# Kernel optimization log

Measured on AMD Instinct MI355X. Metric: run time of the kernel, lower is better.

Reference implementation:

```python
import jax, jax.numpy as jnp
import numpy as np

N_NODES = 50000
N_EDGES = 800000
D = 128
HEADS = 4
HEAD_DIM = D // HEADS
N_LAYERS = 3
NEG_SLOPE = 0.2


def setup_inputs() -> dict:
    key = jax.random.key(0)
    ks = jax.random.split(key, 10)
    x = jax.random.normal(ks[0], (N_NODES, D), dtype=jnp.float32)
    edge_index = jax.random.randint(ks[1], (2, N_EDGES), 0, N_NODES, dtype=jnp.int32)
    s = 1.0 / np.sqrt(D)
    gcn_w = jax.random.normal(ks[2], (N_LAYERS, D, D), dtype=jnp.float32) * s
    gcn_b = jnp.zeros((N_LAYERS, D), dtype=jnp.float32)
    gat_w = jax.random.normal(ks[3], (N_LAYERS, D, D), dtype=jnp.float32) * s
    gat_att_src = jax.random.normal(ks[4], (N_LAYERS, HEADS, HEAD_DIM), dtype=jnp.float32) * s
    gat_att_dst = jax.random.normal(ks[5], (N_LAYERS, HEADS, HEAD_DIM), dtype=jnp.float32) * s
    gat_b = jnp.zeros((N_LAYERS, D), dtype=jnp.float32)
    ln_g = jnp.ones((N_LAYERS, D), dtype=jnp.float32)
    ln_b = jnp.zeros((N_LAYERS, D), dtype=jnp.float32)
    return {"x": x, "edge_index": edge_index, "gcn_w": gcn_w, "gcn_b": gcn_b,
            "gat_w": gat_w, "gat_att_src": gat_att_src, "gat_att_dst": gat_att_dst,
            "gat_b": gat_b, "ln_g": ln_g, "ln_b": ln_b}


def _gcn(x, src, dst, n, w, b):
    # PyG GCNConv: self-loops (already in src/dst), symmetric normalization
    xw = x @ w                                             # [N, D]
    deg = jax.ops.segment_sum(jnp.ones_like(dst, dtype=xw.dtype), dst, num_segments=n)
    dinv = jax.lax.rsqrt(deg)                              # deg >= 1 due to self-loops
    norm = dinv[src] * dinv[dst]                           # [E]
    out = jax.ops.segment_sum(xw[src] * norm[:, None], dst, num_segments=n)
    return out + b


def _gat(x, src, dst, n, w, att_src, att_dst, b):
    # PyG GATConv, concat heads, self-loops already in src/dst
    xw = (x @ w).reshape(n, HEADS, HEAD_DIM)               # [N, H, Dh]
    a_src = (xw * att_src).sum(-1)                         # [N, H]
    a_dst = (xw * att_dst).sum(-1)                         # [N, H]
    e = jax.nn.leaky_relu(a_src[src] + a_dst[dst], NEG_SLOPE)  # [E, H]
    m = jax.ops.segment_max(e, dst, num_segments=n)        # [N, H]
    ee = jnp.exp(e - m[dst])
    z = jax.ops.segment_sum(ee, dst, num_segments=n)       # [N, H]
    alpha = ee / z[dst]                                    # [E, H]
    out = jax.ops.segment_sum(xw[src] * alpha[:, :, None], dst, num_segments=n)
    return out.reshape(n, HEADS * HEAD_DIM) + b


def _layernorm(x, g, b, eps=1e-5):
    mu = x.mean(-1, keepdims=True)
    var = ((x - mu) ** 2).mean(-1, keepdims=True)
    return (x - mu) * jax.lax.rsqrt(var + eps) * g + b


def reference(x, edge_index, gcn_w, gcn_b, gat_w, gat_att_src, gat_att_dst, gat_b, ln_g, ln_b):
    n = x.shape[0]
    loops = jnp.arange(n, dtype=edge_index.dtype)
    src = jnp.concatenate([edge_index[0], loops])
    dst = jnp.concatenate([edge_index[1], loops])
    h = x
    for i in range(N_LAYERS):
        h_gcn = _gcn(h, src, dst, n, gcn_w[i], gcn_b[i])
        h_att = _gat(h_gcn, src, dst, n, gat_w[i], gat_att_src[i], gat_att_dst[i], gat_b[i])
        h = _layernorm(h_att + h_gcn, ln_g[i], ln_b[i])
        h = jax.nn.relu(h)  # dropout is identity in eval mode
    return h
```

## Files before the change

kernel.cpp:

```cpp
#include <hip/hip_runtime.h>

#define NN 50000
#define NE 800000
#define NOUT (NN * 128)
#define PF_TOTAL 100608

typedef unsigned int u32;
typedef unsigned short u16;

__device__ __forceinline__ float bf2f(u16 u) { return __uint_as_float(((u32)u) << 16); }
__device__ __forceinline__ u32 f2bf_u(float f) {
  u32 u = __float_as_uint(f);
  u += 0x7FFFu + ((u >> 16) & 1u);
  return u >> 16;
}
__device__ __forceinline__ u32 pk2(float a, float b) {
  return f2bf_u(a) | (f2bf_u(b) << 16);
}
__device__ __forceinline__ float lo_f(u32 v) { return __uint_as_float(v << 16); }
__device__ __forceinline__ float hi_f(u32 v) { return __uint_as_float(v & 0xFFFF0000u); }
__device__ __forceinline__ float h2f(u16 h) {
  u32 sg = ((u32)h >> 15) & 1u, e = ((u32)h >> 10) & 0x1Fu, mm = (u32)h & 0x3FFu;
  u32 o;
  if (e == 0u) o = sg << 31;
  else if (e == 31u) o = (sg << 31) | 0x7F800000u | (mm << 13);
  else o = (sg << 31) | ((e + 112u) << 23) | (mm << 13);
  return __uint_as_float(o);
}
__device__ __forceinline__ float lrelu(float x) { return x > 0.f ? x : 0.2f * x; }
__device__ __forceinline__ u32 umin32(u32 a, u32 b) { return a < b ? a : b; }

__device__ __forceinline__ float cvt_one(const void* p, int j, u32 fmode) {
  if (fmode == 1u) return ((const float*)p)[j];
  if (fmode == 2u) return h2f(((const u16*)p)[j]);
  return bf2f(((const u16*)p)[j]);
}

__global__ __launch_bounds__(256) void MultiScaleGNN_54769422958784_kernel(
    float* out, float val, int n) {
  int i = blockIdx.x * 256 + threadIdx.x;
  if (i < n) out[i] = val;
}

__global__ __launch_bounds__(64) void detect_kernel(const u32* lng, const int* ei,
                                                    u32* flag) {
  if (threadIdx.x == 0) {
    u32 v0 = lng[0], v1 = lng[1];
    u32 fm;
    if (v0 == 0x3F803F80u && v1 == 0x3F803F80u) fm = 0u;
    else if (v0 == 0x3F800000u && v1 == 0x3F800000u) fm = 1u;
    else if (v0 == 0x3C003C00u && v1 == 0x3C003C00u) fm = 2u;
    else fm = 1u;
    flag[0] = fm;
    flag[1] = ((ei[1] | ei[3] | ei[5] | ei[7]) == 0) ? 1u : 0u;
  }
}

__global__ __launch_bounds__(256) void cvt_x_kernel(const void* in, u32* outh, int n64,
                                                    const u32* flag) {
  u32 fm = flag[0];
  int i = blockIdx.x * 256 + threadIdx.x;
  if (i >= n64) return;
  int node = i >> 6, w = i & 63;
  float a = cvt_one(in, node * 128 + w * 2, fm);
  float b = cvt_one(in, node * 128 + w * 2 + 1, fm);
  outh[i] = pk2(a, b);
}

__global__ __launch_bounds__(256) void cvt_params_kernel(const void* g0, const void* g1,
                                                         const void* g2, const void* g3,
                                                         const void* g4, const void* g5,
                                                         const void* g6, const void* g7,
                                                         float* out, const u32* flag) {
  u32 fm = flag[0];
  int i = blockIdx.x * 256 + threadIdx.x;
  if (i >= PF_TOTAL) return;
  int offs[9] = {0, 49152, 49536, 98688, 99072, 99456, 99840, 100224, 100608};
  const void* ptrs[8] = {g0, g1, g2, g3, g4, g5, g6, g7};
  int r = 0;
  while (i >= offs[r + 1]) r++;
  out[i] = cvt_one(ptrs[r], i - offs[r], fm);
}

__global__ __launch_bounds__(256) void zero1_kernel(u32* a, int n) {
  int i = blockIdx.x * 256 + threadIdx.x;
  if (i < n) a[i] = 0u;
}

__global__ __launch_bounds__(256) void rank_kernel(const int* ei, u32* cnt, u32* rank,
                                                   int e, int n, const u32* flag) {
  int i = blockIdx.x * blockDim.x + threadIdx.x;
  if (i >= e) return;
  int d = flag[1] ? ei[2 * e + 2 * i] : ei[e + i];
  u32 r = 0u;
  if ((u32)d < (u32)n) r = atomicAdd(&cnt[d], 1u);
  rank[i] = r;
}

__device__ __forceinline__ u32 wave_incl_scan(u32 v, int lane) {
#pragma unroll
  for (int off = 1; off < 64; off <<= 1) {
    u32 t = (u32)__shfl_up((int)v, off);
    if (lane >= off) v += t;
  }
  return v;
}

__global__ __launch_bounds__(256) void scan_sum_kernel(const u32* counts, u32* bsums,
                                                       int n) {
  __shared__ u32 ws[4];
  int i = blockIdx.x * 256 + threadIdx.x;
  int lane = threadIdx.x & 63, wid = threadIdx.x >> 6;
  u32 c = (i < n) ? counts[i] : 0u;
#pragma unroll
  for (int off = 32; off; off >>= 1) c += (u32)__shfl_xor((int)c, off);
  if (lane == 0) ws[wid] = c;
  __syncthreads();
  if (threadIdx.x == 0) bsums[blockIdx.x] = ws[0] + ws[1] + ws[2] + ws[3];
}

__global__ __launch_bounds__(256) void scan_bsums_kernel(u32* bsums, u32* rowptr, int nb,
                                                         int n) {
  __shared__ u32 ws[4];
  int tid = threadIdx.x, lane = tid & 63, wid = tid >> 6;
  u32 v = (tid < nb) ? bsums[tid] : 0u;
  u32 incl = wave_incl_scan(v, lane);
  if (lane == 63) ws[wid] = incl;
  __syncthreads();
  u32 wo = 0u;
  for (int w = 0; w < wid; w++) wo += ws[w];
  u32 excl = incl - v + wo;
  if (tid < nb) bsums[tid] = excl;
  if (tid == 0) rowptr[n] = ws[0] + ws[1] + ws[2] + ws[3];
}

__global__ __launch_bounds__(256) void scan_write_kernel(const u32* counts,
                                                         const u32* bsums, u32* rowptr,
                                                         float* dinv, int n) {
  __shared__ u32 ws[4];
  int b = blockIdx.x;
  int i = b * 256 + threadIdx.x;
  int lane = threadIdx.x & 63, wid = threadIdx.x >> 6;
  u32 c = (i < n) ? counts[i] : 0u;
  u32 incl = wave_incl_scan(c, lane);
  if (lane == 63) ws[wid] = incl;
  __syncthreads();
  u32 wo = bsums[b];
  for (int w = 0; w < wid; w++) wo += ws[w];
  u32 excl = incl - c + wo;
  if (i < n) {
    rowptr[i] = excl;
    dinv[i] = rsqrtf((float)(c + 1u));
  }
}

__global__ __launch_bounds__(256) void place_kernel(const int* ei, const u32* rowptr,
                                                    const u32* rank, int* col, int e,
                                                    int n, const u32* flag) {
  int i = blockIdx.x * blockDim.x + threadIdx.x;
  if (i >= e) return;
  u32 em = flag[1];
  int s = em ? ei[2 * i] : ei[i];
  int d = em ? ei[2 * e + 2 * i] : ei[e + i];
  if ((u32)d >= (u32)n) return;
  u32 p = rowptr[d] + rank[i];
  if (p < (u32)e) col[p] = ((u32)s < (u32)n) ? s : 0;
}

__global__ __launch_bounds__(256) void gemm_kernel(const u32* __restrict__ Ah,
                                                   const float* W, u32* __restrict__ Oh,
                                                   const float* dinv, const float* att_s,
                                                   const float* att_d, float* asrc,
                                                   float* adst, int M) {
  __shared__ float As[16][132];
  __shared__ float Bs[16][128];
  int tid = threadIdx.x;
  int row0 = blockIdx.x * 128;
  int tx = tid & 15, ty = tid >> 4;
  int c0 = tx * 8, r0 = ty * 8;
  float acc[8][8];
  for (int i = 0; i < 8; i++)
    for (int j = 0; j < 8; j++) acc[i][j] = 0.f;
  for (int k0 = 0; k0 < 128; k0 += 16) {
    for (int it = 0; it < 2; it++) {
      int r = (tid >> 2) + it * 64;
      int kq = (tid & 3) * 4;
      uint2 av = make_uint2(0u, 0u);
      if (row0 + r < M)
        av = *(const uint2*)(Ah + (size_t)(row0 + r) * 64 + (k0 + kq) / 2);
      As[kq + 0][r] = lo_f(av.x);
      As[kq + 1][r] = hi_f(av.x);
      As[kq + 2][r] = lo_f(av.y);
      As[kq + 3][r] = hi_f(av.y);
    }
    {
      int k = tid >> 4;
      int c8 = (tid & 15) * 8;
      float4 w0 = *(const float4*)(W + (k0 + k) * 128 + c8);
      float4 w1 = *(const float4*)(W + (k0 + k) * 128 + c8 + 4);
      *(float4*)&Bs[k][c8] = w0;
      *(float4*)&Bs[k][c8 + 4] = w1;
    }
    __syncthreads();
#pragma unroll
    for (int kk = 0; kk < 16; kk++) {
      float a[8], b[8];
#pragma unroll
      for (int i = 0; i < 8; i++) a[i] = As[kk][r0 + i];
#pragma unroll
      for (int j = 0; j < 8; j++) b[j] = Bs[kk][c0 + j];
#pragma unroll
      for (int i = 0; i < 8; i++)
#pragma unroll
        for (int j = 0; j < 8; j++) acc[i][j] = fmaf(a[i], b[j], acc[i][j]);
    }
    __syncthreads();
  }
  float ws_[8], wd_[8];
  if (att_s) {
#pragma unroll
    for (int j = 0; j < 8; j++) {
      ws_[j] = att_s[c0 + j];
      wd_[j] = att_d[c0 + j];
    }
  }
  int head = tx >> 2;
  for (int i = 0; i < 8; i++) {
    int r = row0 + r0 + i;
    if (r < M) {
      float sc = (dinv != 0) ? dinv[r] : 1.0f;
      float v0 = acc[i][0] * sc, v1 = acc[i][1] * sc, v2 = acc[i][2] * sc,
            v3 = acc[i][3] * sc;
      float v4 = acc[i][4] * sc, v5 = acc[i][5] * sc, v6 = acc[i][6] * sc,
            v7 = acc[i][7] * sc;
      uint4 p = make_uint4(pk2(v0, v1), pk2(v2, v3), pk2(v4, v5), pk2(v6, v7));
      *(uint4*)(Oh + (size_t)r * 64 + tx * 4) = p;
      if (att_s) {
        float ps = v0 * ws_[0] + v1 * ws_[1] + v2 * ws_[2] + v3 * ws_[3] + v4 * ws_[4] +
                   v5 * ws_[5] + v6 * ws_[6] + v7 * ws_[7];
        float pd = v0 * wd_[0] + v1 * wd_[1] + v2 * wd_[2] + v3 * wd_[3] + v4 * wd_[4] +
                   v5 * wd_[5] + v6 * wd_[6] + v7 * wd_[7];
        ps += __shfl_xor(ps, 1);
        ps += __shfl_xor(ps, 2);
        pd += __shfl_xor(pd, 1);
        pd += __shfl_xor(pd, 2);
        if ((tx & 3) == 0) {
          asrc[(size_t)r * 4 + head] = ps;
          adst[(size_t)r * 4 + head] = pd;
        }
      }
    }
  }
}

__global__ __launch_bounds__(256) void gcn_agg_kernel(const u32* __restrict__ xh,
                                                      const int* col, const u32* rowptr,
                                                      const float* dinv, const float* bias,
                                                      u32* __restrict__ outh, int n) {
  __shared__ int lds_s[8][32];
  int g = threadIdx.x >> 5;
  int l = threadIdx.x & 31;
  int d = blockIdx.x * 8 + g;
  if (d >= n) return;
  u32 start = umin32(rowptr[d], (u32)NE), end = umin32(rowptr[d + 1], (u32)NE);
  float4 acc = make_float4(0.f, 0.f, 0.f, 0.f);
  for (u32 base = start; base < end; base += 32) {
    u32 i = base + l;
    int cnt = (int)umin32(32u, end - base);
    if (i < end) lds_s[g][l] = col[i];
#pragma unroll 4
    for (int j = 0; j < cnt; j++) {
      int s = lds_s[g][j];
      uint2 v = *(const uint2*)(xh + (size_t)s * 64 + l * 2);
      acc.x += lo_f(v.x);
      acc.y += hi_f(v.x);
      acc.z += lo_f(v.y);
      acc.w += hi_f(v.y);
    }
  }
  int c0 = l * 4;
  uint2 sv = *(const uint2*)(xh + (size_t)d * 64 + l * 2);
  float dd = dinv[d];
  float o0 = dd * (acc.x + lo_f(sv.x)) + bias[c0];
  float o1 = dd * (acc.y + hi_f(sv.x)) + bias[c0 + 1];
  float o2 = dd * (acc.z + lo_f(sv.y)) + bias[c0 + 2];
  float o3 = dd * (acc.w + hi_f(sv.y)) + bias[c0 + 3];
  *(uint2*)(outh + (size_t)d * 64 + l * 2) = make_uint2(pk2(o0, o1), pk2(o2, o3));
}

__global__ __launch_bounds__(256) void gat_agg_kernel(
    const u32* __restrict__ xh, const float* a_src4, const float* a_dst4, const int* col,
    const u32* rowptr, const u32* __restrict__ hgcnh, const float* gat_b,
    const float* ln_g, const float* ln_b, u32* __restrict__ outh,
    float* __restrict__ outf, int n) {
  __shared__ u32 lds_s[8][32];
  __shared__ float lds_ee[8][32][4];
  int g = threadIdx.x >> 5;
  int l = threadIdx.x & 31;
  int head4 = l >> 3;
  int d = blockIdx.x * 8 + g;
  if (d >= n) return;
  u32 start = umin32(rowptr[d], (u32)NE), end = umin32(rowptr[d + 1], (u32)NE);
  float4 ad = *(const float4*)(a_dst4 + (size_t)d * 4);
  float4 asl = *(const float4*)(a_src4 + (size_t)d * 4);
  float4 es;
  es.x = lrelu(asl.x + ad.x);
  es.y = lrelu(asl.y + ad.y);
  es.z = lrelu(asl.z + ad.z);
  es.w = lrelu(asl.w + ad.w);
  float4 m = es;
  float4 zp = make_float4(0.f, 0.f, 0.f, 0.f);
  float4 acc = make_float4(0.f, 0.f, 0.f, 0.f);
  for (u32 base = start; base < end; base += 32) {
    u32 i = base + l;
    int cnt = (int)umin32(32u, end - base);
    bool act = i < end;
    float4 lg = make_float4(-1e30f, -1e30f, -1e30f, -1e30f);
    int s = 0;
    if (act) {
      s = col[i];
      float4 a = *(const float4*)(a_src4 + (size_t)s * 4);
      lg.x = lrelu(a.x + ad.x);
      lg.y = lrelu(a.y + ad.y);
      lg.z = lrelu(a.z + ad.z);
      lg.w = lrelu(a.w + ad.w);
    }
    float4 cm = lg;
#pragma unroll
    for (int off = 16; off; off >>= 1) {
      cm.x = fmaxf(cm.x, __shfl_xor(cm.x, off));
      cm.y = fmaxf(cm.y, __shfl_xor(cm.y, off));
      cm.z = fmaxf(cm.z, __shfl_xor(cm.z, off));
      cm.w = fmaxf(cm.w, __shfl_xor(cm.w, off));
    }
    float4 mn;
    mn.x = fmaxf(m.x, cm.x);
    mn.y = fmaxf(m.y, cm.y);
    mn.z = fmaxf(m.z, cm.z);
    mn.w = fmaxf(m.w, cm.w);
    float4 f;
    f.x = __expf(m.x - mn.x);
    f.y = __expf(m.y - mn.y);
    f.z = __expf(m.z - mn.z);
    f.w = __expf(m.w - mn.w);
    m = mn;
    zp.x *= f.x;
    zp.y *= f.y;
    zp.z *= f.z;
    zp.w *= f.w;
    float fsel = (head4 == 0) ? f.x : (head4 == 1) ? f.y : (head4 == 2) ? f.z : f.w;
    acc.x *= fsel;
    acc.y *= fsel;
    acc.z *= fsel;
    acc.w *= fsel;
    if (act) {
      float ex = __expf(lg.x - m.x);
      float ey = __expf(lg.y - m.y);
      float ez = __expf(lg.z - m.z);
      float ew = __expf(lg.w - m.w);
      zp.x += ex;
      zp.y += ey;
      zp.z += ez;
      zp.w += ew;
      lds_s[g][l] = (u32)s;
      *(float4*)&lds_ee[g][l][0] = make_float4(ex, ey, ez, ew);
    }
#pragma unroll 4
    for (int j = 0; j < cnt; j++) {
      u32 sg = lds_s[g][j];
      float w = lds_ee[g][j][head4];
      uint2 v = *(const uint2*)(xh + (size_t)sg * 64 + l * 2);
      acc.x = fmaf(w, lo_f(v.x), acc.x);
      acc.y = fmaf(w, hi_f(v.x), acc.y);
      acc.z = fmaf(w, lo_f(v.y), acc.z);
      acc.w = fmaf(w, hi_f(v.y), acc.w);
    }
  }
  float4 ees;
  ees.x = __expf(es.x - m.x);
  ees.y = __expf(es.y - m.y);
  ees.z = __expf(es.z - m.z);
  ees.w = __expf(es.w - m.w);
#pragma unroll
  for (int off = 16; off; off >>= 1) {
    zp.x += __shfl_xor(zp.x, off);
    zp.y += __shfl_xor(zp.y, off);
    zp.z += __shfl_xor(zp.z, off);
    zp.w += __shfl_xor(zp.w, off);
  }
  zp.x += ees.x;
  zp.y += ees.y;
  zp.z += ees.z;
  zp.w += ees.w;
  float wsel = (head4 == 0) ? ees.x : (head4 == 1) ? ees.y : (head4 == 2) ? ees.z : ees.w;
  float zsel = (head4 == 0) ? zp.x : (head4 == 1) ? zp.y : (head4 == 2) ? zp.z : zp.w;
  int c0 = l * 4;
  uint2 sv = *(const uint2*)(xh + (size_t)d * 64 + l * 2);
  acc.x = fmaf(wsel, lo_f(sv.x), acc.x);
  acc.y = fmaf(wsel, hi_f(sv.x), acc.y);
  acc.z = fmaf(wsel, lo_f(sv.y), acc.z);
  acc.w = fmaf(wsel, hi_f(sv.y), acc.w);
  float rz = 1.0f / zsel;
  uint2 hgv = *(const uint2*)(hgcnh + (size_t)d * 64 + l * 2);
  float t0 = acc.x * rz + gat_b[c0] + lo_f(hgv.x);
  float t1 = acc.y * rz + gat_b[c0 + 1] + hi_f(hgv.x);
  float t2 = acc.z * rz + gat_b[c0 + 2] + lo_f(hgv.y);
  float t3 = acc.w * rz + gat_b[c0 + 3] + hi_f(hgv.y);
  float ssum = t0 + t1 + t2 + t3;
#pragma unroll
  for (int off = 16; off; off >>= 1) ssum += __shfl_xor(ssum, off);
  float mu = ssum * (1.0f / 128.0f);
  float d0 = t0 - mu, d1 = t1 - mu, d2 = t2 - mu, d3 = t3 - mu;
  float vv = d0 * d0 + d1 * d1 + d2 * d2 + d3 * d3;
#pragma unroll
  for (int off = 16; off; off >>= 1) vv += __shfl_xor(vv, off);
  float rstd = rsqrtf(vv * (1.0f / 128.0f) + 1e-5f);
  float o0 = fmaxf(fmaf(d0 * rstd, ln_g[c0], ln_b[c0]), 0.f);
  float o1 = fmaxf(fmaf(d1 * rstd, ln_g[c0 + 1], ln_b[c0 + 1]), 0.f);
  float o2 = fmaxf(fmaf(d2 * rstd, ln_g[c0 + 2], ln_b[c0 + 2]), 0.f);
  float o3 = fmaxf(fmaf(d3 * rstd, ln_g[c0 + 3], ln_b[c0 + 3]), 0.f);
  if (outf) {
    *(float4*)(outf + (size_t)d * 128 + c0) = make_float4(o0, o1, o2, o3);
  } else {
    *(uint2*)(outh + (size_t)d * 64 + l * 2) = make_uint2(pk2(o0, o1), pk2(o2, o3));
  }
}

extern "C" void kernel_launch(void* const* d_in, const int* in_sizes, int n_in,
                              void* d_out, int out_size, void* d_ws, size_t ws_size,
                              hipStream_t stream) {
  const int N = NN, E = NE;
  (void)in_sizes;
  (void)n_in;
  (void)out_size;
  (void)ws_size;

  char* ws = (char*)d_ws;
  size_t off = 0;
  u32* xwh = (u32*)(ws + off);      off += (size_t)N * 64 * 4;
  u32* hbufh = (u32*)(ws + off);    off += (size_t)N * 64 * 4;
  u32* hgcnh = (u32*)(ws + off);    off += (size_t)N * 64 * 4;
  float* asrc = (float*)(ws + off); off += (size_t)N * 4 * 4;
  float* adst = (float*)(ws + off); off += (size_t)N * 4 * 4;
  float* dinv = (float*)(ws + off); off += (size_t)N * 4;
  u32* counts = (u32*)(ws + off);   off += (size_t)N * 4;
  u32* rowptr = (u32*)(ws + off);   off += (size_t)(N + 1) * 4 + 252;
  u32* rank = (u32*)(ws + off);     off += (size_t)E * 4;
  int* col = (int*)(ws + off);      off += (size_t)E * 4;
  float* pf = (float*)(ws + off);   off += (size_t)PF_TOTAL * 4;
  u32* bsums = (u32*)(ws + off);    off += 256 * 4;
  u32* flag = (u32*)(ws + off);     off += 256;

  const int* edge_index = (const int*)d_in[1];
  detect_kernel<<<1, 64, 0, stream>>>((const u32*)d_in[8], edge_index, flag);
  cvt_params_kernel<<<(PF_TOTAL + 255) / 256, 256, 0, stream>>>(
      d_in[2], d_in[3], d_in[4], d_in[5], d_in[6], d_in[7], d_in[8], d_in[9], pf, flag);
  cvt_x_kernel<<<(N * 64 + 255) / 256, 256, 0, stream>>>(d_in[0], hbufh, N * 64, flag);
  zero1_kernel<<<(N + 255) / 256, 256, 0, stream>>>(counts, N);
  rank_kernel<<<(E + 255) / 256, 256, 0, stream>>>(edge_index, counts, rank, E, N, flag);
  {
    int nb = (N + 255) / 256;
    scan_sum_kernel<<<nb, 256, 0, stream>>>(counts, bsums, N);
    scan_bsums_kernel<<<1, 256, 0, stream>>>(bsums, rowptr, nb, N);
    scan_write_kernel<<<nb, 256, 0, stream>>>(counts, bsums, rowptr, dinv, N);
  }
  place_kernel<<<(E + 255) / 256, 256, 0, stream>>>(edge_index, rowptr, rank, col, E, N,
                                                    flag);

  const float* gcn_w = pf + 0;
  const float* gcn_b = pf + 49152;
  const float* gat_w = pf + 49536;
  const float* att_s = pf + 98688;
  const float* att_d = pf + 99072;
  const float* gat_b = pf + 99456;
  const float* ln_g = pf + 99840;
  const float* ln_b = pf + 100224;

  int gblocks = (N + 127) / 128;
  int ablocks = (N + 7) / 8;
  for (int l = 0; l < 3; l++) {
    gemm_kernel<<<gblocks, 256, 0, stream>>>(hbufh, gcn_w + (size_t)l * 16384, xwh, dinv,
                                             (const float*)0, (const float*)0, (float*)0,
                                             (float*)0, N);
    gcn_agg_kernel<<<ablocks, 256, 0, stream>>>(xwh, col, rowptr, dinv, gcn_b + l * 128,
                                                hgcnh, N);
    gemm_kernel<<<gblocks, 256, 0, stream>>>(hgcnh, gat_w + (size_t)l * 16384, xwh,
                                             (const float*)0, att_s + l * 128,
                                             att_d + l * 128, asrc, adst, N);
    gat_agg_kernel<<<ablocks, 256, 0, stream>>>(
        xwh, asrc, adst, col, rowptr, hgcnh, gat_b + l * 128, ln_g + l * 128,
        ln_b + l * 128, hbufh, (l < 2) ? (float*)0 : (float*)d_out, N);
  }
}
```

Before: 563.2 us.

## Replace scalar FMA GEMM with bf16 MFMA kernel using pre-transposed weights

Swaps the LDS-tiled fp32 FMA GEMM for a kernel built on bf16 MFMA 16x16x32 instructions. Activations and packed, transposed bf16 weights are read directly from global memory, with no shared-memory staging. A new setup kernel converts and transposes all six weight matrices once. This targets the ALU-bound six GEMMs, at the cost of rounding the weights to bf16 and relying on the cache to serve repeated weight loads.

```diff
diff --git a/kernel.cpp b/kernel.cpp
--- a/kernel.cpp
+++ b/kernel.cpp
@@ -7,6 +7,9 @@
 
 typedef unsigned int u32;
 typedef unsigned short u16;
+
+typedef __attribute__((ext_vector_type(4))) float f32x4;
+typedef __attribute__((ext_vector_type(8))) short bf16x8;
 
 __device__ __forceinline__ float bf2f(u16 u) { return __uint_as_float(((u32)u) << 16); }
 __device__ __forceinline__ u32 f2bf_u(float f) {
@@ -80,6 +83,20 @@
   int r = 0;
   while (i >= offs[r + 1]) r++;
   out[i] = cvt_one(ptrs[r], i - offs[r], fm);
+}
+
+__global__ __launch_bounds__(256) void cvt_wt_kernel(const float* __restrict__ pf,
+                                                     u32* __restrict__ wt) {
+  int i = blockIdx.x * 256 + threadIdx.x;
+  if (i >= 49152) return;
+  int mat = i >> 13;
+  int rem = i & 8191;
+  int kk = rem >> 7;
+  int n = rem & 127;
+  const float* W = pf + (mat < 3 ? (size_t)mat * 16384 : 49536 + (size_t)(mat - 3) * 16384);
+  float a = W[(2 * kk) * 128 + n];
+  float b = W[(2 * kk + 1) * 128 + n];
+  wt[(size_t)mat * 8192 + n * 64 + kk] = pk2(a, b);
 }
 
 __global__ __launch_bounds__(256) void zero1_kernel(u32* a, int n) {
@@ -167,86 +184,80 @@
   if (p < (u32)e) col[p] = ((u32)s < (u32)n) ? s : 0;
 }
 
-__global__ __launch_bounds__(256) void gemm_kernel(const u32* __restrict__ Ah,
-                                                   const float* W, u32* __restrict__ Oh,
-                                                   const float* dinv, const float* att_s,
-                                                   const float* att_d, float* asrc,
-                                                   float* adst, int M) {
-  __shared__ float As[16][132];
-  __shared__ float Bs[16][128];
+__global__ __launch_bounds__(256) void gemm_mfma_kernel(
+    const u32* __restrict__ Ah, const u32* __restrict__ WTh, u32* __restrict__ Oh,
+    const float* __restrict__ dinv, const float* __restrict__ att_s,
+    const float* __restrict__ att_d, float* __restrict__ asrc,
+    float* __restrict__ adst, int M) {
   int tid = threadIdx.x;
-  int row0 = blockIdx.x * 128;
-  int tx = tid & 15, ty = tid >> 4;
-  int c0 = tx * 8, r0 = ty * 8;
-  float acc[8][8];
-  for (int i = 0; i < 8; i++)
-    for (int j = 0; j < 8; j++) acc[i][j] = 0.f;
-  for (int k0 = 0; k0 < 128; k0 += 16) {
-    for (int it = 0; it < 2; it++) {
-      int r = (tid >> 2) + it * 64;
-      int kq = (tid & 3) * 4;
-      uint2 av = make_uint2(0u, 0u);
-      if (row0 + r < M)
-        av = *(const uint2*)(Ah + (size_t)(row0 + r) * 64 + (k0 + kq) / 2);
-      As[kq + 0][r] = lo_f(av.x);
-      As[kq + 1][r] = hi_f(av.x);
-      As[kq + 2][r] = lo_f(av.y);
-      As[kq + 3][r] = hi_f(av.y);
-    }
-    {
-      int k = tid >> 4;
-      int c8 = (tid & 15) * 8;
-      float4 w0 = *(const float4*)(W + (k0 + k) * 128 + c8);
-      float4 w1 = *(const float4*)(W + (k0 + k) * 128 + c8 + 4);
-      *(float4*)&Bs[k][c8] = w0;
-      *(float4*)&Bs[k][c8 + 4] = w1;
-    }
-    __syncthreads();
-#pragma unroll
-    for (int kk = 0; kk < 16; kk++) {
-      float a[8], b[8];
-#pragma unroll
-      for (int i = 0; i < 8; i++) a[i] = As[kk][r0 + i];
-#pragma unroll
-      for (int j = 0; j < 8; j++) b[j] = Bs[kk][c0 + j];
-#pragma unroll
-      for (int i = 0; i < 8; i++)
-#pragma unroll
-        for (int j = 0; j < 8; j++) acc[i][j] = fmaf(a[i], b[j], acc[i][j]);
-    }
-    __syncthreads();
-  }
-  float ws_[8], wd_[8];
-  if (att_s) {
-#pragma unroll
-    for (int j = 0; j < 8; j++) {
-      ws_[j] = att_s[c0 + j];
-      wd_[j] = att_d[c0 + j];
-    }
-  }
-  int head = tx >> 2;
-  for (int i = 0; i < 8; i++) {
-    int r = row0 + r0 + i;
+  int wave = tid >> 6, lane = tid & 63;
+  int p = lane & 15, g = lane >> 4;
+  int r0 = blockIdx.x * 128 + wave * 32;
+  int ra = r0 + p, rb = r0 + 16 + p;
+  int rac = min(ra, M - 1), rbc = min(rb, M - 1);
+
+  const u32* apA = Ah + (size_t)rac * 64 + g * 4;
+  const u32* apB = Ah + (size_t)rbc * 64 + g * 4;
+  uint4 bA[4], bB[4];
+#pragma unroll
+  for (int k0 = 0; k0 < 4; k0++) {
+    bA[k0] = *(const uint4*)(apA + k0 * 16);
+    bB[k0] = *(const uint4*)(apB + k0 * 16);
+  }
+
+  f32x4 acc0[8], acc1[8];
+#pragma unroll
+  for (int t = 0; t < 8; t++) {
+    acc0[t] = (f32x4)0.f;
+    acc1[t] = (f32x4)0.f;
+  }
+
+  const u32* wp = WTh + p * 64 + g * 4;
+#pragma unroll
+  for (int k0 = 0; k0 < 4; k0++) {
+    bf16x8 fa = __builtin_bit_cast(bf16x8, bA[k0]);
+    bf16x8 fb = __builtin_bit_cast(bf16x8, bB[k0]);
+#pragma unroll
+    for (int t = 0; t < 8; t++) {
+      uint4 af = *(const uint4*)(wp + t * 1024 + k0 * 16);
+      bf16x8 aw = __builtin_bit_cast(bf16x8, af);
+      acc0[t] = __builtin_amdgcn_mfma_f32_16x16x32_bf16(aw, fa, acc0[t], 0, 0, 0);
+      acc1[t] = __builtin_amdgcn_mfma_f32_16x16x32_bf16(aw, fb, acc1[t], 0, 0, 0);
+    }
+  }
+
+#pragma unroll
+  for (int i = 0; i < 2; i++) {
+    int r = r0 + i * 16 + p;
     if (r < M) {
-      float sc = (dinv != 0) ? dinv[r] : 1.0f;
-      float v0 = acc[i][0] * sc, v1 = acc[i][1] * sc, v2 = acc[i][2] * sc,
-            v3 = acc[i][3] * sc;
-      float v4 = acc[i][4] * sc, v5 = acc[i][5] * sc, v6 = acc[i][6] * sc,
-            v7 = acc[i][7] * sc;
-      uint4 p = make_uint4(pk2(v0, v1), pk2(v2, v3), pk2(v4, v5), pk2(v6, v7));
-      *(uint4*)(Oh + (size_t)r * 64 + tx * 4) = p;
+      float sc = dinv ? dinv[r] : 1.0f;
+      u32* orow = Oh + (size_t)r * 64;
+      float hs[4] = {0.f, 0.f, 0.f, 0.f};
+      float hd[4] = {0.f, 0.f, 0.f, 0.f};
+#pragma unroll
+      for (int t = 0; t < 8; t++) {
+        f32x4 v = (i == 0) ? acc0[t] : acc1[t];
+        float v0 = v[0] * sc, v1 = v[1] * sc, v2 = v[2] * sc, v3 = v[3] * sc;
+        *(uint2*)(orow + t * 8 + g * 2) = make_uint2(pk2(v0, v1), pk2(v2, v3));
+        if (att_s) {
+          float4 wsv = *(const float4*)(att_s + t * 16 + g * 4);
+          float4 wdv = *(const float4*)(att_d + t * 16 + g * 4);
+          int h = t >> 1;
+          hs[h] += v0 * wsv.x + v1 * wsv.y + v2 * wsv.z + v3 * wsv.w;
+          hd[h] += v0 * wdv.x + v1 * wdv.y + v2 * wdv.z + v3 * wdv.w;
+        }
+      }
       if (att_s) {
-        float ps = v0 * ws_[0] + v1 * ws_[1] + v2 * ws_[2] + v3 * ws_[3] + v4 * ws_[4] +
-                   v5 * ws_[5] + v6 * ws_[6] + v7 * ws_[7];
-        float pd = v0 * wd_[0] + v1 * wd_[1] + v2 * wd_[2] + v3 * wd_[3] + v4 * wd_[4] +
-                   v5 * wd_[5] + v6 * wd_[6] + v7 * wd_[7];
-        ps += __shfl_xor(ps, 1);
-        ps += __shfl_xor(ps, 2);
-        pd += __shfl_xor(pd, 1);
-        pd += __shfl_xor(pd, 2);
-        if ((tx & 3) == 0) {
-          asrc[(size_t)r * 4 + head] = ps;
-          adst[(size_t)r * 4 + head] = pd;
+#pragma unroll
+        for (int h = 0; h < 4; h++) {
+          hs[h] += __shfl_xor(hs[h], 16);
+          hs[h] += __shfl_xor(hs[h], 32);
+          hd[h] += __shfl_xor(hd[h], 16);
+          hd[h] += __shfl_xor(hd[h], 32);
+        }
+        if (g == 0) {
+          *(float4*)(asrc + (size_t)r * 4) = make_float4(hs[0], hs[1], hs[2], hs[3]);
+          *(float4*)(adst + (size_t)r * 4) = make_float4(hd[0], hd[1], hd[2], hd[3]);
         }
       }
     }
@@ -448,6 +459,7 @@
   u32* rank = (u32*)(ws + off);     off += (size_t)E * 4;
   int* col = (int*)(ws + off);      off += (size_t)E * 4;
   float* pf = (float*)(ws + off);   off += (size_t)PF_TOTAL * 4;
+  u32* wt = (u32*)(ws + off);       off += (size_t)49152 * 4;
   u32* bsums = (u32*)(ws + off);    off += 256 * 4;
   u32* flag = (u32*)(ws + off);     off += 256;
 
@@ -455,6 +467,7 @@
   detect_kernel<<<1, 64, 0, stream>>>((const u32*)d_in[8], edge_index, flag);
   cvt_params_kernel<<<(PF_TOTAL + 255) / 256, 256, 0, stream>>>(
       d_in[2], d_in[3], d_in[4], d_in[5], d_in[6], d_in[7], d_in[8], d_in[9], pf, flag);
+  cvt_wt_kernel<<<(49152 + 255) / 256, 256, 0, stream>>>(pf, wt);
   cvt_x_kernel<<<(N * 64 + 255) / 256, 256, 0, stream>>>(d_in[0], hbufh, N * 64, flag);
   zero1_kernel<<<(N + 255) / 256, 256, 0, stream>>>(counts, N);
   rank_kernel<<<(E + 255) / 256, 256, 0, stream>>>(edge_index, counts, rank, E, N, flag);
@@ -467,11 +480,9 @@
   place_kernel<<<(E + 255) / 256, 256, 0, stream>>>(edge_index, rowptr, rank, col, E, N,
                                                     flag);
 
-  const float* gcn_w = pf + 0;
-  const float* gcn_b = pf + 49152;
-  const float* gat_w = pf + 49536;
   const float* att_s = pf + 98688;
   const float* att_d = pf + 99072;
+  const float* gcn_b = pf + 49152;
   const float* gat_b = pf + 99456;
   const float* ln_g = pf + 99840;
   const float* ln_b = pf + 100224;
@@ -479,14 +490,14 @@
   int gblocks = (N + 127) / 128;
   int ablocks = (N + 7) / 8;
   for (int l = 0; l < 3; l++) {
-    gemm_kernel<<<gblocks, 256, 0, stream>>>(hbufh, gcn_w + (size_t)l * 16384, xwh, dinv,
-                                             (const float*)0, (const float*)0, (float*)0,
-                                             (float*)0, N);
+    gemm_mfma_kernel<<<gblocks, 256, 0, stream>>>(
+        hbufh, wt + (size_t)l * 8192, xwh, dinv, (const float*)0, (const float*)0,
+        (float*)0, (float*)0, N);
     gcn_agg_kernel<<<ablocks, 256, 0, stream>>>(xwh, col, rowptr, dinv, gcn_b + l * 128,
                                                 hgcnh, N);
-    gemm_kernel<<<gblocks, 256, 0, stream>>>(hgcnh, gat_w + (size_t)l * 16384, xwh,
-                                             (const float*)0, att_s + l * 128,
-                                             att_d + l * 128, asrc, adst, N);
+    gemm_mfma_kernel<<<gblocks, 256, 0, stream>>>(
+        hgcnh, wt + (size_t)(3 + l) * 8192, xwh, (const float*)0, att_s + l * 128,
+        att_d + l * 128, asrc, adst, N);
     gat_agg_kernel<<<ablocks, 256, 0, stream>>>(
         xwh, asrc, adst, col, rowptr, hgcnh, gat_b + l * 128, ln_g + l * 128,
         ln_b + l * 128, hbufh, (l < 2) ? (float*)0 : (float*)d_out, N);
```

Measured after the change: 476.3 us. -15.4%, faster.
